# Performance work log

Hardware: AMD Instinct MI355X
Metric: run time of the kernel (lower is better)

Reference implementation:

```python
import jax, jax.numpy as jnp
import numpy as np

NBINS = 29
NODES = 5


def setup_inputs() -> dict:
    key = jax.random.key(0)
    ks = jax.random.split(key, 9)
    B, Tq, Td, V, H = 64, 32, 4096, 100000, 300
    sentence = jax.random.randint(ks[0], (B, Td), 0, V)
    query_sentence = jax.random.randint(ks[1], (B, Tq), 0, V)
    query_idf = jax.random.uniform(ks[2], (B, Tq), jnp.float32)
    emb = jax.random.normal(ks[3], (V, H), jnp.float32)
    w1 = jax.random.uniform(ks[4], (NBINS + 1, NODES), jnp.float32, -0.1, 0.1)
    b1 = jnp.zeros((NODES,), jnp.float32)
    w2 = jax.random.uniform(ks[5], (NODES, 1), jnp.float32, -0.1, 0.1)
    b2 = jnp.zeros((1,), jnp.float32)
    gate_w = jax.random.uniform(ks[6], (1,), jnp.float32, -0.01, 0.01)
    out_w = jax.random.normal(ks[7], (1, 1), jnp.float32) * 0.1
    out_b = jnp.zeros((1,), jnp.float32)
    return dict(sentence=sentence, query_sentence=query_sentence, query_idf=query_idf,
                emb=emb, w1=w1, b1=b1, w2=w2, b2=b2, gate_w=gate_w, out_w=out_w, out_b=out_b)


def reference(sentence, query_sentence, query_idf, emb, w1, b1, w2, b2, gate_w, out_w, out_b):
    B, Td = sentence.shape
    Tq = query_sentence.shape[1]
    q_mask = (query_sentence != 0).astype(jnp.float32)  # (B,Tq)
    d_mask = (sentence != 0).astype(jnp.float32)        # (B,Td)
    qx = emb[query_sentence]                            # (B,Tq,H)
    dx = emb[sentence]                                  # (B,Td,H)
    q_norm = jnp.sqrt(jnp.sum(qx * qx, -1) + 1e-7)[:, :, None] + 1e-7
    d_norm = jnp.sqrt(jnp.sum(dx * dx, -1) + 1e-7)[:, None, :] + 1e-7
    sim = jnp.einsum('bqh,bdh->bqd', qx, dx) / q_norm / d_norm  # (B,Tq,Td)
    sim = sim + (1.0 - d_mask)[:, None, :] * 1e7  # push masked doc positions out of all bins
    # Histogram: original does nbins cumulative (sim < ub) passes then a cumulative
    # subtraction; equivalent per-element bin index + one scatter-add pass.
    ubs = jnp.linspace(-1.0, 1.0, NBINS + 1)[1:]
    idx = jnp.searchsorted(ubs, sim, side='right')  # bin j <=> ub[j-1] <= sim < ub[j]; NBINS = out-of-range
    rows = jnp.arange(B * Tq)[:, None]
    counts = jnp.zeros((B * Tq, NBINS), jnp.float32).at[rows, idx.reshape(B * Tq, Td)].add(1.0, mode='drop')
    counts = counts.reshape(B, Tq, NBINS)
    exact = jnp.sum((sim > 0.999) & (sim < 1.001), axis=-1).astype(jnp.float32)  # exact-match bin
    hist = jnp.log(jnp.concatenate([counts, exact[..., None]], axis=-1) + 1.0)   # histType == 'LCH'
    ffw = jnp.tanh(jnp.tanh(hist @ w1 + b1) @ w2 + b2)[..., 0]  # (B,Tq)
    # gateType == 'IDF': Linear(1,1,bias=False) on idf, masked softmax over query terms
    gate_logits = query_idf * gate_w[0] + (1.0 - q_mask) * -1e7
    w = jax.nn.softmax(gate_logits, axis=1)
    x = jnp.sum(w * ffw, axis=-1, keepdims=True)  # (B,1)
    return x * out_w[0, 0] + out_b
```

## Files before the change

### kernel.cpp

```cpp
#include <hip/hip_runtime.h>
#include <hip/hip_bf16.h>
#include <math.h>

#define B_    64
#define TQ    32
#define TD    4096
#define HDIM  300
#define NB    29
#define NFEAT 30
#define NKT   19
#define THREADS 256
#define NCH   2
#define DPB   128
#define RDEP  8
#define NBUCK 1024
#define QF_SLOTS (NKT * 2 * 64)
#define QF_F4    (QF_SLOTS / 2)
#define QF_BYTES (QF_SLOTS * 8)

typedef _Float16 half4 __attribute__((ext_vector_type(4)));
typedef float    f32x4 __attribute__((ext_vector_type(4)));

__device__ __forceinline__ float ubf(int k) {
    return (float)(-1.0 + (2.0 * (double)(k + 1)) / 29.0);
}

__device__ __forceinline__ void bin_one(float sim, unsigned* s_hist, int q) {
    if (sim > 0.999f && sim < 1.001f) {
        atomicAdd(&s_hist[q * NFEAT + 28], 1u);
        atomicAdd(&s_hist[q * NFEAT + 29], 1u);
    } else {
        int idx = (int)((sim + 1.0f) * 14.5f);
        idx = idx < 0 ? 0 : (idx > NB ? NB : idx);
        while (idx < NB && sim >= ubf(idx)) ++idx;
        while (idx > 0 && sim < ubf(idx - 1)) --idx;
        if (idx < NB) atomicAdd(&s_hist[q * NFEAT + idx], 1u);
    }
}

__global__ void k_sort(const int* __restrict__ sent, int* __restrict__ sorted) {
    const int b = blockIdx.x;
    const int t = threadIdx.x;
    const int lane = t & 63, wv = t >> 6;
    __shared__ unsigned cnt[NBUCK];
    __shared__ unsigned wtot[4];
    for (int i = t; i < NBUCK; i += 256) cnt[i] = 0u;
    __syncthreads();
    int tk[16];
#pragma unroll
    for (int j = 0; j < 16; ++j) tk[j] = sent[b * TD + j * 256 + t];
#pragma unroll
    for (int j = 0; j < 16; ++j) atomicAdd(&cnt[(unsigned)tk[j] >> 7], 1u);
    __syncthreads();
    unsigned c0 = cnt[t * 4], c1 = cnt[t * 4 + 1], c2 = cnt[t * 4 + 2], c3 = cnt[t * 4 + 3];
    unsigned s = c0 + c1 + c2 + c3;
    unsigned v = s;
#pragma unroll
    for (int d = 1; d < 64; d <<= 1) {
        unsigned n = __shfl_up(v, d, 64);
        if (lane >= d) v += n;
    }
    if (lane == 63) wtot[wv] = v;
    __syncthreads();
    unsigned wbase = 0;
    for (int w = 0; w < wv; ++w) wbase += wtot[w];
    const unsigned base = wbase + v - s;
    __syncthreads();
    cnt[t * 4]     = base;
    cnt[t * 4 + 1] = base + c0;
    cnt[t * 4 + 2] = base + c0 + c1;
    cnt[t * 4 + 3] = base + c0 + c1 + c2;
    __syncthreads();
#pragma unroll
    for (int j = 0; j < 16; ++j) {
        unsigned pos = atomicAdd(&cnt[(unsigned)tk[j] >> 7], 1u);
        sorted[b * TD + pos] = tk[j];
    }
}

__global__ void k_qfrag(const int* __restrict__ qsent, const float* __restrict__ emb,
                        _Float16* __restrict__ qf, float* __restrict__ invq,
                        unsigned* __restrict__ ghist) {
    const int b = blockIdx.x;
    const int t = threadIdx.x;
    const int row = t & 31, seg = t >> 5;
    __shared__ float pn[8][TQ];
    for (int i = t; i < TQ * NFEAT; i += 256) ghist[b * TQ * NFEAT + i] = 0u;
    const int tok = qsent[b * TQ + row];
    const float* p = emb + (size_t)tok * HDIM;
    _Float16* qfb = qf + (size_t)b * (QF_SLOTS * 4);
    float n = 0.f;
#pragma unroll
    for (int i = 0; i < 10; ++i) {
        const int jf = seg * 10 + i;
        if (jf < 76) {
            const int kg = jf * 4;
            float4 v = make_float4(0.f, 0.f, 0.f, 0.f);
            if (kg < 297) v = *(const float4*)(p + kg);
            n = fmaf(v.x, v.x, n); n = fmaf(v.y, v.y, n);
            n = fmaf(v.z, v.z, n); n = fmaf(v.w, v.w, n);
            half4 h = {(_Float16)v.x, (_Float16)v.y, (_Float16)v.z, (_Float16)v.w};
            const int kt = jf >> 2, g = jf & 3;
            const int slot = (kt * 2 + (row >> 4)) * 64 + (row & 15) + 16 * g;
            *(half4*)&qfb[slot * 4] = h;
        }
    }
    pn[seg][row] = n;
    __syncthreads();
    if (t < TQ) {
        float s = ((pn[0][t] + pn[1][t]) + (pn[2][t] + pn[3][t]))
                + ((pn[4][t] + pn[5][t]) + (pn[6][t] + pn[7][t]));
        invq[b * TQ + t] = 1.0f / (sqrtf(s + 1e-7f) + 1e-7f);
    }
}

__global__ __launch_bounds__(THREADS) void k_main(
        const int* __restrict__ sorted, const float* __restrict__ emb,
        const _Float16* __restrict__ qf, const float* __restrict__ invq,
        unsigned* __restrict__ ghist) {
    __shared__ __align__(16) _Float16 afr[QF_SLOTS * 4];
    __shared__ float    s_iq[TQ];
    __shared__ unsigned s_hist[TQ * NFEAT];

    const int b    = blockIdx.x >> 5;
    const int d0   = (blockIdx.x & 31) * DPB;
    const int tid  = threadIdx.x;
    const int wid  = tid >> 6;
    const int lane = tid & 63;

    const int g4   = lane >> 4;
    const int r16  = lane & 15;

    int tok[NCH];
    const float* bp[NCH];
#pragma unroll
    for (int ch = 0; ch < NCH; ++ch) {
        tok[ch] = sorted[b * TD + d0 + ch * 64 + wid * 16 + r16];
        bp[ch]  = emb + (size_t)tok[ch] * HDIM + g4 * 4;
    }

    auto ldBg = [&](int g) -> float4 {
        const int ch = g / NKT, kt = g - ch * NKT;
        if (kt == 18 && g4 == 3) return make_float4(0.f, 0.f, 0.f, 0.f);
        return *(const float4*)(bp[ch] + kt * 16);
    };

    float4 pre[RDEP];
#pragma unroll
    for (int p = 0; p < RDEP; ++p) pre[p] = ldBg(p);

    for (int i = tid; i < TQ * NFEAT; i += THREADS) s_hist[i] = 0u;
    {
        const float4* qfp = (const float4*)(qf + (size_t)b * (QF_SLOTS * 4));
        float4* afp = (float4*)afr;
        for (int i = tid; i < QF_F4; i += THREADS) afp[i] = qfp[i];
    }
    if (tid < TQ) s_iq[tid] = invq[b * TQ + tid];
    __syncthreads();

#pragma unroll
    for (int ch = 0; ch < NCH; ++ch) {
        f32x4 acc0 = {0.f, 0.f, 0.f, 0.f};
        f32x4 acc1 = {0.f, 0.f, 0.f, 0.f};
        float nd = 0.f;
#pragma unroll
        for (int kt = 0; kt < NKT; ++kt) {
            const int g = ch * NKT + kt;
            float4 v = pre[g % RDEP];
            if (g + RDEP < NCH * NKT) pre[g % RDEP] = ldBg(g + RDEP);
            nd = fmaf(v.x, v.x, nd); nd = fmaf(v.y, v.y, nd);
            nd = fmaf(v.z, v.z, nd); nd = fmaf(v.w, v.w, nd);
            half4 hb = {(_Float16)v.x, (_Float16)v.y, (_Float16)v.z, (_Float16)v.w};
            half4 a0 = *(const half4*)&afr[((kt * 2 + 0) * 64 + lane) * 4];
            half4 a1 = *(const half4*)&afr[((kt * 2 + 1) * 64 + lane) * 4];
            acc0 = __builtin_amdgcn_mfma_f32_16x16x16f16(a0, hb, acc0, 0, 0, 0);
            acc1 = __builtin_amdgcn_mfma_f32_16x16x16f16(a1, hb, acc1, 0, 0, 0);
        }
        float t = nd;
        t += __shfl_xor(t, 16, 64);
        t += __shfl_xor(t, 32, 64);
        const float idv = 1.0f / (sqrtf(t + 1e-7f) + 1e-7f);
        if (tok[ch] != 0) {
#pragma unroll
            for (int r = 0; r < 4; ++r) {
                const int q0 = g4 * 4 + r;
                bin_one(acc0[r] * s_iq[q0] * idv, s_hist, q0);
                const int q1 = 16 + g4 * 4 + r;
                bin_one(acc1[r] * s_iq[q1] * idv, s_hist, q1);
            }
        }
    }
    __syncthreads();
    for (int i = tid; i < TQ * NFEAT; i += THREADS) {
        unsigned v = s_hist[i];
        if (v) atomicAdd(&ghist[b * TQ * NFEAT + i], v);
    }
}

__global__ void k_finish(const unsigned* __restrict__ ghist,
                         const int* __restrict__ qsent, const float* __restrict__ idf,
                         const float* __restrict__ w1, const float* __restrict__ b1,
                         const float* __restrict__ w2, const float* __restrict__ b2,
                         const float* __restrict__ gw, const float* __restrict__ ow,
                         const float* __restrict__ ob, float* __restrict__ out) {
    int b = blockIdx.x;
    int lane = threadIdx.x;
    float ffw = 0.f;
    float logit = -3.0e38f;
    if (lane < TQ) {
        const unsigned* h = ghist + (b * TQ + lane) * NFEAT;
        float f[NFEAT];
        for (int k = 0; k < NFEAT; ++k) f[k] = logf((float)h[k] + 1.0f);
        float s2 = b2[0];
        for (int n = 0; n < 5; ++n) {
            float s = b1[n];
            for (int k = 0; k < NFEAT; ++k) s = fmaf(f[k], w1[k * 5 + n], s);
            s2 = fmaf(tanhf(s), w2[n], s2);
        }
        ffw = tanhf(s2);
        int qt = qsent[b * TQ + lane];
        logit = idf[b * TQ + lane] * gw[0] + (qt == 0 ? -1e7f : 0.f);
    }
    float m = logit;
#pragma unroll
    for (int t = 1; t < 64; t <<= 1) m = fmaxf(m, __shfl_xor(m, t, 64));
    float e = expf(logit - m);
    float se = e, sw = e * ffw;
#pragma unroll
    for (int t = 1; t < 64; t <<= 1) {
        se += __shfl_xor(se, t, 64);
        sw += __shfl_xor(sw, t, 64);
    }
    if (lane == 0) out[b] = (sw / se) * ow[0] + ob[0];
}

extern "C" void kernel_launch(void* const* d_in, const int* in_sizes, int n_in,
                              void* d_out, int out_size, void* d_ws, size_t ws_size,
                              hipStream_t stream) {
    const int*   sent  = (const int*)d_in[0];
    const int*   qsent = (const int*)d_in[1];
    const float* idf   = (const float*)d_in[2];
    const float* emb   = (const float*)d_in[3];
    const float* w1    = (const float*)d_in[4];
    const float* b1    = (const float*)d_in[5];
    const float* w2    = (const float*)d_in[6];
    const float* b2    = (const float*)d_in[7];
    const float* gw    = (const float*)d_in[8];
    const float* ow    = (const float*)d_in[9];
    const float* ob    = (const float*)d_in[10];
    float* out = (float*)d_out;

    char* ws = (char*)d_ws;
    unsigned*  ghist  = (unsigned*)ws;
    _Float16*  qfrag  = (_Float16*)(ws + (256 << 10));
    float*     invq   = (float*)(ws + (256 << 10) + (size_t)B_ * QF_BYTES);
    int*       sorted = (int*)(ws + (256 << 10) + (size_t)B_ * QF_BYTES
                               + (size_t)B_ * TQ * 4);

    k_sort<<<B_, 256, 0, stream>>>(sent, sorted);
    k_qfrag<<<B_, 256, 0, stream>>>(qsent, emb, qfrag, invq, ghist);
    k_main<<<B_ * (TD / DPB), THREADS, 0, stream>>>(sorted, emb, qfrag, invq, ghist);
    k_finish<<<B_, 64, 0, stream>>>(ghist, qsent, idf, w1, b1, w2, b2, gw, ow, ob, out);
}
```

Baseline: 80.76 us.

## Pre-convert embedding table to padded fp16 and gather half-width rows in main kernel

Adds a kernel that converts the whole fp32 embedding table into a padded fp16 copy (row stride 304) in workspace on every call. The main kernel then gathers document rows as half4 directly, with no per-load conversion or tail masking. The aim is to halve the bytes moved by the random row gathers in the similarity stage. The cost is a full-table read plus write on each call. The new path only runs when the workspace is large enough, otherwise the fp32 kernel is used. Document norms are now computed from fp16-rounded values.

```diff
diff --git a/kernel.cpp b/kernel.cpp
--- a/kernel.cpp
+++ b/kernel.cpp
@@ -14,6 +14,8 @@
 #define DPB   128
 #define RDEP  8
 #define NBUCK 1024
+#define VROW  100000
+#define H16   304
 #define QF_SLOTS (NKT * 2 * 64)
 #define QF_F4    (QF_SLOTS / 2)
 #define QF_BYTES (QF_SLOTS * 8)
@@ -35,6 +37,22 @@
         while (idx < NB && sim >= ubf(idx)) ++idx;
         while (idx > 0 && sim < ubf(idx - 1)) --idx;
         if (idx < NB) atomicAdd(&s_hist[q * NFEAT + idx], 1u);
+    }
+}
+
+__global__ void k_conv(const float* __restrict__ emb, _Float16* __restrict__ emb16) {
+    const long long total = (long long)VROW * (H16 / 4);
+    for (long long c = (long long)blockIdx.x * blockDim.x + threadIdx.x;
+         c < total; c += (long long)gridDim.x * blockDim.x) {
+        const int r = (int)(c / (H16 / 4));
+        const int j = (int)(c - (long long)r * (H16 / 4));
+        const int kg = j * 4;
+        half4 h = {(_Float16)0.f, (_Float16)0.f, (_Float16)0.f, (_Float16)0.f};
+        if (kg < HDIM) {
+            float4 v = *(const float4*)(emb + (size_t)r * HDIM + kg);
+            h = (half4){(_Float16)v.x, (_Float16)v.y, (_Float16)v.z, (_Float16)v.w};
+        }
+        *(half4*)(emb16 + (size_t)r * H16 + kg) = h;
     }
 }
 
@@ -114,7 +132,90 @@
     }
 }
 
-__global__ __launch_bounds__(THREADS) void k_main(
+__global__ __launch_bounds__(THREADS) void k_main_f16(
+        const int* __restrict__ sorted, const _Float16* __restrict__ emb16,
+        const _Float16* __restrict__ qf, const float* __restrict__ invq,
+        unsigned* __restrict__ ghist) {
+    __shared__ __align__(16) _Float16 afr[QF_SLOTS * 4];
+    __shared__ float    s_iq[TQ];
+    __shared__ unsigned s_hist[TQ * NFEAT];
+
+    const int b    = blockIdx.x >> 5;
+    const int d0   = (blockIdx.x & 31) * DPB;
+    const int tid  = threadIdx.x;
+    const int wid  = tid >> 6;
+    const int lane = tid & 63;
+
+    const int g4   = lane >> 4;
+    const int r16  = lane & 15;
+
+    int tok[NCH];
+    const _Float16* bp[NCH];
+#pragma unroll
+    for (int ch = 0; ch < NCH; ++ch) {
+        tok[ch] = sorted[b * TD + d0 + ch * 64 + wid * 16 + r16];
+        bp[ch]  = emb16 + (size_t)tok[ch] * H16 + g4 * 4;
+    }
+
+    auto ldBg = [&](int g) -> half4 {
+        const int ch = g / NKT, kt = g - ch * NKT;
+        return *(const half4*)(bp[ch] + kt * 16);
+    };
+
+    half4 pre[RDEP];
+#pragma unroll
+    for (int p = 0; p < RDEP; ++p) pre[p] = ldBg(p);
+
+    for (int i = tid; i < TQ * NFEAT; i += THREADS) s_hist[i] = 0u;
+    {
+        const float4* qfp = (const float4*)(qf + (size_t)b * (QF_SLOTS * 4));
+        float4* afp = (float4*)afr;
+        for (int i = tid; i < QF_F4; i += THREADS) afp[i] = qfp[i];
+    }
+    if (tid < TQ) s_iq[tid] = invq[b * TQ + tid];
+    __syncthreads();
+
+#pragma unroll
+    for (int ch = 0; ch < NCH; ++ch) {
+        f32x4 acc0 = {0.f, 0.f, 0.f, 0.f};
+        f32x4 acc1 = {0.f, 0.f, 0.f, 0.f};
+        float nd = 0.f;
+#pragma unroll
+        for (int kt = 0; kt < NKT; ++kt) {
+            const int g = ch * NKT + kt;
+            half4 hb = pre[g % RDEP];
+            if (g + RDEP < NCH * NKT) pre[g % RDEP] = ldBg(g + RDEP);
+            const float x0 = (float)hb[0], x1 = (float)hb[1];
+            const float x2 = (float)hb[2], x3 = (float)hb[3];
+            nd = fmaf(x0, x0, nd); nd = fmaf(x1, x1, nd);
+            nd = fmaf(x2, x2, nd); nd = fmaf(x3, x3, nd);
+            half4 a0 = *(const half4*)&afr[((kt * 2 + 0) * 64 + lane) * 4];
+            half4 a1 = *(const half4*)&afr[((kt * 2 + 1) * 64 + lane) * 4];
+            acc0 = __builtin_amdgcn_mfma_f32_16x16x16f16(a0, hb, acc0, 0, 0, 0);
+            acc1 = __builtin_amdgcn_mfma_f32_16x16x16f16(a1, hb, acc1, 0, 0, 0);
+        }
+        float t = nd;
+        t += __shfl_xor(t, 16, 64);
+        t += __shfl_xor(t, 32, 64);
+        const float idv = 1.0f / (sqrtf(t + 1e-7f) + 1e-7f);
+        if (tok[ch] != 0) {
+#pragma unroll
+            for (int r = 0; r < 4; ++r) {
+                const int q0 = g4 * 4 + r;
+                bin_one(acc0[r] * s_iq[q0] * idv, s_hist, q0);
+                const int q1 = 16 + g4 * 4 + r;
+                bin_one(acc1[r] * s_iq[q1] * idv, s_hist, q1);
+            }
+        }
+    }
+    __syncthreads();
+    for (int i = tid; i < TQ * NFEAT; i += THREADS) {
+        unsigned v = s_hist[i];
+        if (v) atomicAdd(&ghist[b * TQ * NFEAT + i], v);
+    }
+}
+
+__global__ __launch_bounds__(THREADS) void k_main_f32(
         const int* __restrict__ sorted, const float* __restrict__ emb,
         const _Float16* __restrict__ qf, const float* __restrict__ invq,
         unsigned* __restrict__ ghist) {
@@ -127,7 +228,6 @@
     const int tid  = threadIdx.x;
     const int wid  = tid >> 6;
     const int lane = tid & 63;
-
     const int g4   = lane >> 4;
     const int r16  = lane & 15;
 
@@ -138,13 +238,11 @@
         tok[ch] = sorted[b * TD + d0 + ch * 64 + wid * 16 + r16];
         bp[ch]  = emb + (size_t)tok[ch] * HDIM + g4 * 4;
     }
-
     auto ldBg = [&](int g) -> float4 {
         const int ch = g / NKT, kt = g - ch * NKT;
         if (kt == 18 && g4 == 3) return make_float4(0.f, 0.f, 0.f, 0.f);
         return *(const float4*)(bp[ch] + kt * 16);
     };
-
     float4 pre[RDEP];
 #pragma unroll
     for (int p = 0; p < RDEP; ++p) pre[p] = ldBg(p);
@@ -256,9 +354,17 @@
     float*     invq   = (float*)(ws + (256 << 10) + (size_t)B_ * QF_BYTES);
     int*       sorted = (int*)(ws + (256 << 10) + (size_t)B_ * QF_BYTES
                                + (size_t)B_ * TQ * 4);
+    const size_t emb16_off = 4u << 20;
+    _Float16*  emb16  = (_Float16*)(ws + emb16_off);
+    const size_t need = emb16_off + (size_t)VROW * H16 * 2;
 
     k_sort<<<B_, 256, 0, stream>>>(sent, sorted);
     k_qfrag<<<B_, 256, 0, stream>>>(qsent, emb, qfrag, invq, ghist);
-    k_main<<<B_ * (TD / DPB), THREADS, 0, stream>>>(sorted, emb, qfrag, invq, ghist);
+    if (ws_size >= need) {
+        k_conv<<<2048, 256, 0, stream>>>(emb, emb16);
+        k_main_f16<<<B_ * (TD / DPB), THREADS, 0, stream>>>(sorted, emb16, qfrag, invq, ghist);
+    } else {
+        k_main_f32<<<B_ * (TD / DPB), THREADS, 0, stream>>>(sorted, emb, qfrag, invq, ghist);
+    }
     k_finish<<<B_, 64, 0, stream>>>(ghist, qsent, idf, w1, b1, w2, b2, gw, ow, ob, out);
 }
```

Result: slower. 123.0 us (+52.3%).
